# Performance work log

Hardware: AMD Instinct MI355X
Metric: run time of the kernel (lower is better)

The kernel has to match this reference:

```python
import jax, jax.numpy as jnp
import numpy as np

B, S, D = 2, 2048, 2048
H, HKV, DH = 32, 8, 64
WIN = 1024  # sliding_window
SCALE = 1.0 / np.sqrt(DH)
NEG_INF = -1e30


def setup_inputs() -> dict:
    key = jax.random.key(0)
    ks = jax.random.split(key, 6)
    w = 0.02
    inp = {
        "hidden_states": jax.random.normal(ks[0], (B, S, D), jnp.float32),
        "Wq": jax.random.normal(ks[1], (D, D), jnp.float32) * w,
        "bq": jnp.zeros((D,), jnp.float32),
        "Wk": jax.random.normal(ks[2], (HKV * DH, D), jnp.float32) * w,
        "bk": jnp.zeros((HKV * DH,), jnp.float32),
        "Wv": jax.random.normal(ks[3], (HKV * DH, D), jnp.float32) * w,
        "bv": jnp.zeros((HKV * DH,), jnp.float32),
        "Wo": jax.random.normal(ks[4], (D, D), jnp.float32) * w,
        "bo": jnp.zeros((D,), jnp.float32),
        # reset_parameters (default init): 1 / logspace(0, 7, H, base=2)
        "alibi_slopes": 1.0 / jnp.exp2(jnp.linspace(0.0, 7.0, H)).astype(jnp.float32),
    }
    return inp


def reference(hidden_states, Wq, bq, Wk, bk, Wv, bv, Wo, bo, alibi_slopes):
    x = hidden_states
    q = (x @ Wq.T + bq).reshape(B, S, H, DH).transpose(0, 2, 1, 3)      # [B,H,S,DH]
    k = (x @ Wk.T + bk).reshape(B, S, HKV, DH).transpose(0, 2, 1, 3)    # [B,HKV,S,DH]
    v = (x @ Wv.T + bv).reshape(B, S, HKV, DH).transpose(0, 2, 1, 3)
    # GQA: each kv head serves H//HKV consecutive query heads
    group = H // HKV
    k = jnp.repeat(k, group, axis=1)  # [B,H,S,DH]
    v = jnp.repeat(v, group, axis=1)

    scores = jnp.einsum("bhqd,bhkd->bhqk", q, k) * SCALE  # [B,H,S,S]
    i = jnp.arange(S)[:, None]
    j = jnp.arange(S)[None, :]
    rel = (j - i).astype(jnp.float32)  # <= 0 for attended past positions
    # ALiBi: slope * (j - i) -> linear penalty on distance
    bias = alibi_slopes[:, None, None] * rel  # [H,S,S]
    mask = (j <= i) & ((i - j) < WIN)  # [S,S]
    scores = jnp.where(mask[None, None], scores + bias[None], NEG_INF)
    probs = jax.nn.softmax(scores, axis=-1)
    out = jnp.einsum("bhqk,bhkd->bhqd", probs, v)  # [B,H,S,DH]
    out = out.transpose(0, 2, 1, 3).reshape(B, S, D)
    return out @ Wo.T + bo
```

## Files before the change

kernel.cpp:

```cpp
#include <hip/hip_runtime.h>
#include <hip/hip_bf16.h>
#include <stdint.h>
#include <type_traits>

typedef unsigned short ushort_t;
typedef __bf16 bf16x8 __attribute__((ext_vector_type(8)));
typedef __bf16 bf16x4 __attribute__((ext_vector_type(4)));
typedef short s16x4 __attribute__((ext_vector_type(4)));
typedef unsigned short u16x8 __attribute__((ext_vector_type(8)));
typedef float f32x4 __attribute__((ext_vector_type(4)));

#define MFMA_BF16(a, b, c) __builtin_amdgcn_mfma_f32_16x16x32_bf16((a), (b), (c), 0, 0, 0)

#define GLD_LDS(gptr, lptr) \
    __builtin_amdgcn_global_load_lds((const __attribute__((address_space(1))) void*)(gptr), \
                                     (__attribute__((address_space(3))) void*)(lptr), 16, 0, 0)

static __device__ __forceinline__ float bf2f(__hip_bfloat16 x) { return __bfloat162float(x); }
static __device__ __forceinline__ ushort_t f2bfbits(float f) {
    __hip_bfloat16 h = __float2bfloat16(f);
    return *(ushort_t*)&h;
}

static __device__ __forceinline__ f32x4 MFMA16(bf16x4 a, bf16x4 b, f32x4 c) {
#if __has_builtin(__builtin_amdgcn_mfma_f32_16x16x16_bf16)
    return __builtin_amdgcn_mfma_f32_16x16x16_bf16(a, b, c, 0, 0, 0);
#elif __has_builtin(__builtin_amdgcn_mfma_f32_16x16x16bf16_1k)
    union { bf16x4 b4; s16x4 s4; } ua, ub;
    ua.b4 = a; ub.b4 = b;
    return __builtin_amdgcn_mfma_f32_16x16x16bf16_1k(ua.s4, ub.s4, c, 0, 0, 0);
#else
    const bf16x4 z = {(__bf16)0.f, (__bf16)0.f, (__bf16)0.f, (__bf16)0.f};
    bf16x8 a8 = __builtin_shufflevector(a, z, 0, 1, 2, 3, 4, 5, 6, 7);
    bf16x8 b8 = __builtin_shufflevector(b, z, 0, 1, 2, 3, 4, 5, 6, 7);
    return MFMA_BF16(a8, b8, c);
#endif
}

static __device__ __forceinline__ bf16x4 pack4(float a, float b, float c, float d) {
    union { ushort4 u; bf16x4 v; } r;
    r.u = make_ushort4(f2bfbits(a), f2bfbits(b), f2bfbits(c), f2bfbits(d));
    return r.v;
}

template <typename T>
static __device__ __forceinline__ void storeT(T* p, float v);
template <>
__device__ __forceinline__ void storeT<float>(float* p, float v) { *p = v; }
template <>
__device__ __forceinline__ void storeT<__hip_bfloat16>(__hip_bfloat16* p, float v) {
    *p = __float2bfloat16(v);
}

__global__ void detect_kernel(const ushort_t* __restrict__ X,
                              const void* bq, const void* bk, const void* bv,
                              const void* bo, const void* slopes,
                              int* flag, float* slopesF, float* bqF,
                              float* bkF, float* bvF, float* boF) {
    __shared__ int cnt_s;
    if (threadIdx.x == 0) cnt_s = 0;
    __syncthreads();
    int cnt = 0;
    for (int i = threadIdx.x; i < 8192; i += 256) {
        ushort_t u = X[2 * i];
        int ex = (u >> 7) & 0xFF;
        if (ex >= 0xC0) cnt++;
    }
    for (int off = 1; off < 64; off <<= 1) cnt += __shfl_xor(cnt, off);
    if ((threadIdx.x & 63) == 0) atomicAdd(&cnt_s, cnt);
    __syncthreads();
    const bool f32 = cnt_s > 100;
    if (threadIdx.x == 0) *flag = f32 ? 1 : 0;
    auto conv = [&](const void* src, float* dst, int n) {
        for (int i = threadIdx.x; i < n; i += 256)
            dst[i] = f32 ? ((const float*)src)[i]
                         : __bfloat162float(((const __hip_bfloat16*)src)[i]);
    };
    conv(bq, bqF, 2048);
    conv(bk, bkF, 512);
    conv(bv, bvF, 512);
    conv(bo, boF, 2048);
    conv(slopes, slopesF, 32);
}

__global__ __launch_bounds__(256) void cvt_kernel(const int* __restrict__ flag,
                                                  const void* __restrict__ src,
                                                  ushort_t* __restrict__ dst, int n4) {
    const bool f32 = (*flag == 1);
    const int stride = gridDim.x * 256;
    for (int i = blockIdx.x * 256 + threadIdx.x; i < n4; i += stride) {
        if (f32) {
            float4 f = ((const float4*)src)[i];
            ((ushort4*)dst)[i] =
                make_ushort4(f2bfbits(f.x), f2bfbits(f.y), f2bfbits(f.z), f2bfbits(f.w));
        } else {
            ((ushort4*)dst)[i] = ((const ushort4*)src)[i];
        }
    }
}

__device__ __forceinline__ void stage_tile(const __hip_bfloat16* __restrict__ M, int K,
                                           int k0, ushort_t* lds, int tid) {
    const int wave = tid >> 6, lane = tid & 63;
    const int srow = lane >> 3;
    const int scol = ((lane & 7) ^ srow) * 8;
#pragma unroll
    for (int t = 0; t < 4; ++t) {
        const int chunk = wave * 4 + t;
        GLD_LDS((const ushort_t*)M + (size_t)(chunk * 8 + srow) * K + k0 + scol,
                lds + chunk * 512);
    }
}

__device__ __forceinline__ void stage_tile(const float* __restrict__ M, int K,
                                           int k0, ushort_t* lds, int tid) {
#pragma unroll
    for (int q = 0; q < 8; ++q) {
        const int idx = q * 256 + tid;
        const int row = idx >> 4;
        const int c4 = (idx & 15) * 4;
        float4 f = *(const float4*)(M + (size_t)row * K + k0 + c4);
        const int dcol = (((c4 >> 3) ^ (row & 7)) * 8) + (c4 & 7);
        *(ushort4*)(lds + row * 64 + dcol) =
            make_ushort4(f2bfbits(f.x), f2bfbits(f.y), f2bfbits(f.z), f2bfbits(f.w));
    }
}

template <typename TA, typename TW, typename TC>
__device__ __forceinline__ void gemm_tile(const TA* __restrict__ A,
                                          const TW* __restrict__ W,
                                          const float* __restrict__ biasF,
                                          TC* __restrict__ C, int K, int ldc) {
    __shared__ __align__(16) ushort_t As[128 * 64];
    __shared__ __align__(16) ushort_t Bs[128 * 64];
    const int tid = threadIdx.x;
    const int wave = tid >> 6, lane = tid & 63;
    const int quad = lane >> 4, l15 = lane & 15;
    const int wm = (wave >> 1) * 64, wn = (wave & 1) * 64;
    const int sw = l15 & 7;

    f32x4 acc[4][4];
#pragma unroll
    for (int i = 0; i < 4; ++i)
#pragma unroll
        for (int j = 0; j < 4; ++j) acc[i][j] = {0.f, 0.f, 0.f, 0.f};

    for (int k0 = 0; k0 < K; k0 += 64) {
        stage_tile(A, K, k0, As, tid);
        stage_tile(W, K, k0, Bs, tid);
        __syncthreads();
#pragma unroll
        for (int kk = 0; kk < 2; ++kk) {
            const int chs = ((kk * 4 + quad) ^ sw) * 8;
            bf16x8 af[4], bfr[4];
#pragma unroll
            for (int mi = 0; mi < 4; ++mi)
                af[mi] = *(const bf16x8*)(As + (wm + mi * 16 + l15) * 64 + chs);
#pragma unroll
            for (int ni = 0; ni < 4; ++ni)
                bfr[ni] = *(const bf16x8*)(Bs + (wn + ni * 16 + l15) * 64 + chs);
#pragma unroll
            for (int mi = 0; mi < 4; ++mi)
#pragma unroll
                for (int ni = 0; ni < 4; ++ni)
                    acc[mi][ni] = MFMA_BF16(af[mi], bfr[ni], acc[mi][ni]);
        }
        __syncthreads();
    }
#pragma unroll
    for (int mi = 0; mi < 4; ++mi) {
#pragma unroll
        for (int ni = 0; ni < 4; ++ni) {
            const int col = wn + ni * 16 + l15;
            const float bv = biasF[col];
#pragma unroll
            for (int r = 0; r < 4; ++r) {
                const int row = wm + mi * 16 + quad * 4 + r;
                storeT(C + (size_t)row * ldc + col, acc[mi][ni][r] + bv);
            }
        }
    }
}

__global__ __launch_bounds__(256, 2) void qkv_fast(
    const __hip_bfloat16* __restrict__ X,
    const __hip_bfloat16* __restrict__ Wq, const __hip_bfloat16* __restrict__ Wk,
    const __hip_bfloat16* __restrict__ Wv, const float* __restrict__ bqF,
    const float* __restrict__ bkF, const float* __restrict__ bvF,
    __hip_bfloat16* __restrict__ Qb, __hip_bfloat16* __restrict__ Kb,
    __hip_bfloat16* __restrict__ Vb) {
    const int nt = blockIdx.x, mt = blockIdx.y;
    const __hip_bfloat16* W;
    const float* bias;
    __hip_bfloat16* C;
    int ldc, colbase;
    if (nt < 16)      { W = Wq; bias = bqF; C = Qb; ldc = 2048; colbase = nt * 128; }
    else if (nt < 20) { W = Wk; bias = bkF; C = Kb; ldc = 512;  colbase = (nt - 16) * 128; }
    else              { W = Wv; bias = bvF; C = Vb; ldc = 512;  colbase = (nt - 20) * 128; }
    gemm_tile(X + (size_t)mt * 128 * 2048, W + (size_t)colbase * 2048, bias + colbase,
              C + (size_t)mt * 128 * ldc + colbase, 2048, ldc);
}

__global__ __launch_bounds__(256, 2) void oproj_fast(
    const __hip_bfloat16* __restrict__ A, const __hip_bfloat16* __restrict__ Wo,
    const float* __restrict__ boF, float* __restrict__ C) {
    gemm_tile(A + (size_t)blockIdx.y * 128 * 2048,
              Wo + (size_t)blockIdx.x * 128 * 2048, boF + blockIdx.x * 128,
              C + (size_t)blockIdx.y * 128 * 2048 + blockIdx.x * 128, 2048, 2048);
}

__global__ __launch_bounds__(256) void vtrans_kernel(const ushort_t* __restrict__ Vb,
                                                     ushort_t* __restrict__ Vt) {
    const int blk = blockIdx.x;
    const int bh = blk >> 6;
    const int sc = blk & 63;
    const int tid = threadIdx.x;
    const int dh = tid & 63;
    const int s0 = sc * 32 + (tid >> 6) * 8;
    const int b = bh >> 3, hkv = bh & 7;
    u16x8 vv;
#pragma unroll
    for (int e = 0; e < 8; ++e)
        vv[e] = Vb[((size_t)(b * 2048 + s0 + e)) * 512 + hkv * 64 + dh];
    *(u16x8*)(Vt + ((size_t)(bh * 64 + dh)) * 2048 + s0) = vv;
}

template <bool F32>
__global__ __launch_bounds__(256, 2) void qkv_kernel(
    const int* __restrict__ flag, const void* __restrict__ Xv,
    const void* __restrict__ Wqv, const void* __restrict__ Wkv,
    const void* __restrict__ Wvv, const float* __restrict__ bqF,
    const float* __restrict__ bkF, const float* __restrict__ bvF,
    __hip_bfloat16* __restrict__ Qb, __hip_bfloat16* __restrict__ Kb,
    __hip_bfloat16* __restrict__ Vb) {
    if ((*flag == 1) != F32) return;
    using T = typename std::conditional<F32, float, __hip_bfloat16>::type;
    const T* X = (const T*)Xv;
    const int nt = blockIdx.x, mt = blockIdx.y;
    const T* W;
    const float* bias;
    __hip_bfloat16* C;
    int ldc, colbase;
    if (nt < 16)      { W = (const T*)Wqv; bias = bqF; C = Qb; ldc = 2048; colbase = nt * 128; }
    else if (nt < 20) { W = (const T*)Wkv; bias = bkF; C = Kb; ldc = 512;  colbase = (nt - 16) * 128; }
    else              { W = (const T*)Wvv; bias = bvF; C = Vb; ldc = 512;  colbase = (nt - 20) * 128; }
    gemm_tile(X + (size_t)mt * 128 * 2048, W + (size_t)colbase * 2048, bias + colbase,
              C + (size_t)mt * 128 * ldc + colbase, 2048, ldc);
}

template <bool F32>
__global__ __launch_bounds__(256, 2) void oproj_kernel(
    const int* __restrict__ flag, const __hip_bfloat16* __restrict__ A,
    const void* __restrict__ Wov, const float* __restrict__ boF,
    float* __restrict__ C) {
    if ((*flag == 1) != F32) return;
    using T = typename std::conditional<F32, float, __hip_bfloat16>::type;
    gemm_tile(A + (size_t)blockIdx.y * 128 * 2048,
              (const T*)Wov + (size_t)blockIdx.x * 128 * 2048, boF + blockIdx.x * 128,
              C + (size_t)blockIdx.y * 128 * 2048 + blockIdx.x * 128, 2048, 2048);
}

__global__ __launch_bounds__(256, 4) void attn4_kernel(
    const __hip_bfloat16* __restrict__ Qg, const __hip_bfloat16* __restrict__ Kg,
    const ushort_t* __restrict__ Vt, const float* __restrict__ slopesF,
    __hip_bfloat16* __restrict__ Og) {
    constexpr int S = 2048, WIN = 1024;
    constexpr float LOG2E = 1.44269504f;
    constexpr float SCALE2 = 0.125f * LOG2E;
    constexpr float NEGBIG = -3e38f;
    __shared__ __align__(16) ushort_t K0s[64 * 64];
    __shared__ __align__(16) ushort_t V0s[64 * 64];
    __shared__ __align__(16) ushort_t K1s[64 * 64];
    __shared__ __align__(16) ushort_t V1s[64 * 64];

    const int p = blockIdx.x;
    const int xcd = p & 7;
    const int slot = p >> 3;
    const int bh = (slot >> 7) * 8 + xcd;
    const int h2 = (slot >> 5) & 3;
    const int qt = slot & 31;
    const int b = bh >> 3, hkv = bh & 7;
    const int h = hkv * 4 + h2;
    const int i0 = qt * 64;

    const int tid = threadIdx.x;
    const int wave = tid >> 6, lane = tid & 63;
    const int quad = lane >> 4, l15 = lane & 15;
    const int jl = lane >> 3, cc = lane & 7;
    const float slope2 = slopesF[h] * LOG2E;

    const ushort_t* kbase = (const ushort_t*)Kg + (size_t)(b * S) * 512 + hkv * 64;
    const ushort_t* vbase = Vt + ((size_t)bh * 64) * 2048;

    auto stage = [&](int j0, ushort_t* Ks, ushort_t* Vs) {
        const int row0 = wave * 16;
#pragma unroll
        for (int t = 0; t < 2; ++t) {
            const int r = row0 + t * 8 + jl;
            GLD_LDS(kbase + (size_t)(j0 + r) * 512 + ((cc ^ (r & 7)) * 8),
                    Ks + (row0 + t * 8) * 64);
            GLD_LDS(vbase + (size_t)r * 2048 + j0 + ((cc ^ (r & 7)) * 8),
                    Vs + (row0 + t * 8) * 64);
        }
    };

    const int i = i0 + wave * 16 + l15;
    const __hip_bfloat16* qbase = Qg + ((size_t)(b * S + i)) * 2048 + h * 64;
    bf16x8 aq0 = *(const bf16x8*)(qbase + quad * 8);
    bf16x8 aq1 = *(const bf16x8*)(qbase + 32 + quad * 8);

    f32x4 oaccT[4];
#pragma unroll
    for (int ni = 0; ni < 4; ++ni) oaccT[ni] = {0.f, 0.f, 0.f, 0.f};
    float m_i = -1e30f, l_i = 0.f;

    auto compute = [&](int j0, const ushort_t* Ks, const ushort_t* Vs, bool masked) {
        f32x4 st[4];
#pragma unroll
        for (int ni = 0; ni < 4; ++ni) st[ni] = {0.f, 0.f, 0.f, 0.f};
#pragma unroll
        for (int kk = 0; kk < 2; ++kk) {
            const bf16x8 aqk = kk ? aq1 : aq0;
#pragma unroll
            for (int ni = 0; ni < 4; ++ni) {
                const int row = ni * 16 + l15;
                bf16x8 kf = *(const bf16x8*)(Ks + row * 64 + ((kk * 4 + quad) ^ (row & 7)) * 8);
                st[ni] = MFMA_BF16(kf, aqk, st[ni]);
            }
        }
        float sv[4][4];
#pragma unroll
        for (int ni = 0; ni < 4; ++ni)
#pragma unroll
            for (int r = 0; r < 4; ++r) {
                const int rel = (j0 + ni * 16 + quad * 4 + r) - i;
                sv[ni][r] = fmaf(st[ni][r], SCALE2, slope2 * (float)rel);
            }
        if (masked) {
#pragma unroll
            for (int ni = 0; ni < 4; ++ni)
#pragma unroll
                for (int r = 0; r < 4; ++r) {
                    const int rel = (j0 + ni * 16 + quad * 4 + r) - i;
                    if (!((unsigned)(-rel) < (unsigned)WIN)) sv[ni][r] = NEGBIG;
                }
        }
        float mx = sv[0][0];
#pragma unroll
        for (int ni = 0; ni < 4; ++ni)
#pragma unroll
            for (int r = 0; r < 4; ++r) mx = fmaxf(mx, sv[ni][r]);
        mx = fmaxf(mx, __shfl_xor(mx, 16));
        mx = fmaxf(mx, __shfl_xor(mx, 32));
        const float mn = fmaxf(m_i, mx);
        const float alpha = exp2f(m_i - mn);
        m_i = mn;
        float pv[4][4];
        float rs = 0.f;
#pragma unroll
        for (int ni = 0; ni < 4; ++ni)
#pragma unroll
            for (int r = 0; r < 4; ++r) {
                pv[ni][r] = exp2f(sv[ni][r] - mn);
                rs += pv[ni][r];
            }
        rs += __shfl_xor(rs, 16);
        rs += __shfl_xor(rs, 32);
        l_i = l_i * alpha + rs;
#pragma unroll
        for (int ni = 0; ni < 4; ++ni)
#pragma unroll
            for (int r = 0; r < 4; ++r) oaccT[ni][r] *= alpha;
        bf16x4 pf[4];
#pragma unroll
        for (int c = 0; c < 4; ++c) pf[c] = pack4(pv[c][0], pv[c][1], pv[c][2], pv[c][3]);
#pragma unroll
        for (int ni = 0; ni < 4; ++ni) {
            const int row = ni * 16 + l15;
#pragma unroll
            for (int c = 0; c < 4; ++c) {
                const int cj = c * 2 + (quad >> 1);
                bf16x4 vf = *(const bf16x4*)(Vs + row * 64 + ((cj ^ (row & 7)) * 8) +
                                             (quad & 1) * 4);
                oaccT[ni] = MFMA16(vf, pf[c], oaccT[ni]);
            }
        }
    };

    const int jt_lo = (i0 - WIN + 1) > 0 ? ((i0 - WIN + 1) >> 6) : 0;
    int jt = jt_lo;
    stage(jt * 64, K0s, V0s);
    for (;;) {
        __syncthreads();
        if (jt < qt) stage((jt + 1) * 64, K1s, V1s);
        compute(jt * 64, K0s, V0s, (jt == qt) || (qt - jt >= 16));
        if (++jt > qt) break;
        __syncthreads();
        if (jt < qt) stage((jt + 1) * 64, K0s, V0s);
        compute(jt * 64, K1s, V1s, (jt == qt) || (qt - jt >= 16));
        if (++jt > qt) break;
    }
    const float inv = 1.0f / l_i;
    __hip_bfloat16* obase = Og + ((size_t)(b * S + i)) * 2048 + h * 64;
#pragma unroll
    for (int ni = 0; ni < 4; ++ni) {
        ushort4 o4 = make_ushort4(f2bfbits(oaccT[ni][0] * inv), f2bfbits(oaccT[ni][1] * inv),
                                  f2bfbits(oaccT[ni][2] * inv), f2bfbits(oaccT[ni][3] * inv));
        *(ushort4*)((ushort_t*)obase + ni * 16 + quad * 4) = o4;
    }
}

__global__ __launch_bounds__(256, 2) void attn_kernel(
    const __hip_bfloat16* __restrict__ Qg, const __hip_bfloat16* __restrict__ Kg,
    const __hip_bfloat16* __restrict__ Vg, const float* __restrict__ slopesF,
    __hip_bfloat16* __restrict__ Og) {
    constexpr int S = 2048, WIN = 1024;
    constexpr float SCALE = 0.125f;
    constexpr float LOG2E = 1.44269504f;
    __shared__ __align__(16) ushort_t P_lds[64 * 72];
    __shared__ __align__(16) ushort_t Vts[64 * 72];

    const int tile = blockIdx.x;
    const int qt = tile & 31;
    const int h = (tile >> 5) & 31;
    const int b = tile >> 10;
    const int i0 = qt * 64;
    const int hkv = h >> 2;
    const int tid = threadIdx.x;
    const int wave = tid >> 6, lane = tid & 63;
    const int quad = lane >> 4, l15 = lane & 15;
    const float slope = slopesF[h];

    const int qrow = i0 + wave * 16 + l15;
    const __hip_bfloat16* qbase = Qg + ((size_t)(b * S + qrow)) * 2048 + h * 64;
    bf16x8 aq[2];
    aq[0] = *(const bf16x8*)(qbase + quad * 8);
    aq[1] = *(const bf16x8*)(qbase + 32 + quad * 8);

    f32x4 oacc[4];
#pragma unroll
    for (int ni = 0; ni < 4; ++ni) oacc[ni] = {0.f, 0.f, 0.f, 0.f};
    float m_i[4], l_i[4];
#pragma unroll
    for (int r = 0; r < 4; ++r) { m_i[r] = -1e30f; l_i[r] = 0.f; }

    const int jt_lo = (i0 - WIN + 1) > 0 ? ((i0 - WIN + 1) >> 6) : 0;
    for (int jt = jt_lo; jt <= qt; ++jt) {
        const int j0 = jt * 64;
#pragma unroll
        for (int it = 0; it < 2; ++it) {
            const int j = it * 32 + (tid >> 3);
            const int dh0 = (tid & 7) * 8;
            u16x8 vv = *(const u16x8*)(Vg + ((size_t)(b * S + j0 + j)) * 512 + hkv * 64 + dh0);
#pragma unroll
            for (int e = 0; e < 8; ++e) Vts[(dh0 + e) * 72 + j] = vv[e];
        }
        f32x4 sacc[4];
#pragma unroll
        for (int ni = 0; ni < 4; ++ni) sacc[ni] = {0.f, 0.f, 0.f, 0.f};
#pragma unroll
        for (int kk = 0; kk < 2; ++kk) {
#pragma unroll
            for (int ni = 0; ni < 4; ++ni) {
                bf16x8 bkf = *(const bf16x8*)(Kg + ((size_t)(b * S + j0 + ni * 16 + l15)) * 512 +
                                              hkv * 64 + kk * 32 + quad * 8);
                sacc[ni] = MFMA_BF16(aq[kk], bkf, sacc[ni]);
            }
        }
#pragma unroll
        for (int r = 0; r < 4; ++r) {
            const int i = i0 + wave * 16 + quad * 4 + r;
            float sv[4];
            float rowmax = -1e30f;
#pragma unroll
            for (int ni = 0; ni < 4; ++ni) {
                const int j = j0 + ni * 16 + l15;
                float s = sacc[ni][r] * SCALE + slope * (float)(j - i);
                const bool valid = (j <= i) && ((i - j) < WIN);
                s = valid ? s : -1e30f;
                sv[ni] = s;
                rowmax = fmaxf(rowmax, s);
            }
#pragma unroll
            for (int off = 1; off < 16; off <<= 1)
                rowmax = fmaxf(rowmax, __shfl_xor(rowmax, off));
            const float mn = fmaxf(m_i[r], rowmax);
            const float alpha = exp2f((m_i[r] - mn) * LOG2E);
            float rowsum = 0.f;
#pragma unroll
            for (int ni = 0; ni < 4; ++ni) {
                const float p = (sv[ni] > -1e29f) ? exp2f((sv[ni] - mn) * LOG2E) : 0.f;
                P_lds[(wave * 16 + quad * 4 + r) * 72 + ni * 16 + l15] = f2bfbits(p);
                rowsum += p;
            }
#pragma unroll
            for (int off = 1; off < 16; off <<= 1) rowsum += __shfl_xor(rowsum, off);
            l_i[r] = l_i[r] * alpha + rowsum;
            m_i[r] = mn;
#pragma unroll
            for (int ni = 0; ni < 4; ++ni) oacc[ni][r] *= alpha;
        }
        __syncthreads();
#pragma unroll
        for (int kk = 0; kk < 2; ++kk) {
            bf16x8 ap = *(const bf16x8*)(P_lds + (wave * 16 + l15) * 72 + kk * 32 + quad * 8);
#pragma unroll
            for (int ni = 0; ni < 4; ++ni) {
                bf16x8 bvf = *(const bf16x8*)(Vts + (ni * 16 + l15) * 72 + kk * 32 + quad * 8);
                oacc[ni] = MFMA_BF16(ap, bvf, oacc[ni]);
            }
        }
        __syncthreads();
    }
#pragma unroll
    for (int ni = 0; ni < 4; ++ni) {
#pragma unroll
        for (int r = 0; r < 4; ++r) {
            const int srow = i0 + wave * 16 + quad * 4 + r;
            const float v = oacc[ni][r] / l_i[r];
            Og[((size_t)(b * S + srow)) * 2048 + h * 64 + ni * 16 + l15] = __float2bfloat16(v);
        }
    }
}

extern "C" void kernel_launch(void* const* d_in, const int* in_sizes, int n_in,
                              void* d_out, int out_size, void* d_ws, size_t ws_size,
                              hipStream_t stream) {
    (void)in_sizes; (void)n_in; (void)out_size;
    const void* X  = d_in[0];
    const void* Wq = d_in[1];
    const void* bq = d_in[2];
    const void* Wk = d_in[3];
    const void* bk = d_in[4];
    const void* Wv = d_in[5];
    const void* bv = d_in[6];
    const void* Wo = d_in[7];
    const void* bo = d_in[8];
    const void* sl = d_in[9];
    float* outp = (float*)d_out;

    char* ws = (char*)d_ws;
    const size_t SZ_X  = (size_t)4096 * 2048 * 2;
    const size_t SZ_WQ = (size_t)2048 * 2048 * 2;
    const size_t SZ_WK = (size_t)512 * 2048 * 2;
    const size_t SZ_Q  = SZ_X;
    const size_t SZ_K  = (size_t)4096 * 512 * 2;
    const size_t FAST_NEED = SZ_X + SZ_WQ + 2 * SZ_WK + SZ_Q + 2 * SZ_K + 65536;

    if (ws_size >= FAST_NEED) {
        size_t o = 0;
        __hip_bfloat16* Xb  = (__hip_bfloat16*)(ws + o); o += SZ_X;
        __hip_bfloat16* Wqb = (__hip_bfloat16*)(ws + o); o += SZ_WQ;
        __hip_bfloat16* Wkb = (__hip_bfloat16*)(ws + o); o += SZ_WK;
        __hip_bfloat16* Wvb = (__hip_bfloat16*)(ws + o); o += SZ_WK;
        __hip_bfloat16* Qb  = (__hip_bfloat16*)(ws + o); o += SZ_Q;
        __hip_bfloat16* Kb  = (__hip_bfloat16*)(ws + o); o += SZ_K;
        __hip_bfloat16* Vb  = (__hip_bfloat16*)(ws + o); o += SZ_K;
        __hip_bfloat16* Ab  = Xb;
        __hip_bfloat16* Wob = Wqb;
        ushort_t*       Vtg = (ushort_t*)Wkb;
        int*   flag    = (int*)(ws + o);
        float* slopesF = (float*)(ws + o + 1024);
        float* bqF     = (float*)(ws + o + 4096);
        float* bkF     = bqF + 2048;
        float* bvF     = bkF + 512;
        float* boF     = bvF + 512;

        detect_kernel<<<1, 256, 0, stream>>>((const ushort_t*)X, bq, bk, bv, bo, sl,
                                             flag, slopesF, bqF, bkF, bvF, boF);
        cvt_kernel<<<2048, 256, 0, stream>>>(flag, X,  (ushort_t*)Xb,  4096 * 2048 / 4);
        cvt_kernel<<<2048, 256, 0, stream>>>(flag, Wq, (ushort_t*)Wqb, 2048 * 2048 / 4);
        cvt_kernel<<<512,  256, 0, stream>>>(flag, Wk, (ushort_t*)Wkb, 512 * 2048 / 4);
        cvt_kernel<<<512,  256, 0, stream>>>(flag, Wv, (ushort_t*)Wvb, 512 * 2048 / 4);
        qkv_fast<<<dim3(24, 32), 256, 0, stream>>>(Xb, Wqb, Wkb, Wvb, bqF, bkF, bvF,
                                                   Qb, Kb, Vb);
        vtrans_kernel<<<1024, 256, 0, stream>>>((const ushort_t*)Vb, Vtg);
        cvt_kernel<<<2048, 256, 0, stream>>>(flag, Wo, (ushort_t*)Wob, 2048 * 2048 / 4);
        attn4_kernel<<<dim3(2048), 256, 0, stream>>>(Qb, Kb, Vtg, slopesF, Ab);
        oproj_fast<<<dim3(16, 32), 256, 0, stream>>>(Ab, Wob, boF, outp);
    } else {
        const size_t MB = 1024 * 1024;
        __hip_bfloat16* Qb = (__hip_bfloat16*)(ws);
        __hip_bfloat16* Kb = (__hip_bfloat16*)(ws + 16 * MB);
        __hip_bfloat16* Vb = (__hip_bfloat16*)(ws + 20 * MB);
        __hip_bfloat16* Ab = (__hip_bfloat16*)(ws + 24 * MB);
        int*   flag    = (int*)(ws + 40 * MB);
        float* slopesF = (float*)(ws + 40 * MB + 1024);
        float* bqF     = (float*)(ws + 40 * MB + 4096);
        float* bkF     = bqF + 2048;
        float* bvF     = bkF + 512;
        float* boF     = bvF + 512;

        detect_kernel<<<1, 256, 0, stream>>>((const ushort_t*)X, bq, bk, bv, bo, sl,
                                             flag, slopesF, bqF, bkF, bvF, boF);
        qkv_kernel<false><<<dim3(24, 32), 256, 0, stream>>>(flag, X, Wq, Wk, Wv,
                                                            bqF, bkF, bvF, Qb, Kb, Vb);
        qkv_kernel<true><<<dim3(24, 32), 256, 0, stream>>>(flag, X, Wq, Wk, Wv,
                                                           bqF, bkF, bvF, Qb, Kb, Vb);
        attn_kernel<<<dim3(2048), 256, 0, stream>>>(Qb, Kb, Vb, slopesF, Ab);
        oproj_kernel<false><<<dim3(16, 32), 256, 0, stream>>>(flag, Ab, Wo, boF, outp);
        oproj_kernel<true><<<dim3(16, 32), 256, 0, stream>>>(flag, Ab, Wo, boF, outp);
    }
}
```

Before: 337.8 us.

## Use 256x256 eight-wave ping-pong GEMM tiles for QKV and output projections

```diff
diff --git a/kernel.cpp b/kernel.cpp
--- a/kernel.cpp
+++ b/kernel.cpp
@@ -15,6 +15,38 @@
 #define GLD_LDS(gptr, lptr) \
     __builtin_amdgcn_global_load_lds((const __attribute__((address_space(1))) void*)(gptr), \
                                      (__attribute__((address_space(3))) void*)(lptr), 16, 0, 0)
+
+#define WAIT_VM(n) asm volatile("s_waitcnt vmcnt(" #n ")" ::: "memory")
+#define WAIT_LGKM0 asm volatile("s_waitcnt lgkmcnt(0)" ::: "memory")
+#define SCHED0 __builtin_amdgcn_sched_barrier(0)
+#define SBAR __builtin_amdgcn_s_barrier()
+
+#define PH_SYNC()      \
+    do {               \
+        SCHED0;        \
+        SBAR;          \
+        WAIT_LGKM0;    \
+        SCHED0;        \
+    } while (0)
+#define PH_END() \
+    do {         \
+        SCHED0;  \
+        SBAR;    \
+    } while (0)
+
+#define MFMA_QUAD(M0, N0)                                                               \
+    do {                                                                                \
+        __builtin_amdgcn_s_setprio(1);                                                  \
+        _Pragma("unroll") for (int mi_ = 0; mi_ < 4; ++mi_) {                           \
+            _Pragma("unroll") for (int ni_ = 0; ni_ < 2; ++ni_) {                       \
+                _Pragma("unroll") for (int kk_ = 0; kk_ < 2; ++kk_) {                   \
+                    acc[(M0) + mi_][(N0) + ni_] = MFMA_BF16(                            \
+                        af[mi_][kk_], bfr[(N0) + ni_][kk_], acc[(M0) + mi_][(N0) + ni_]); \
+                }                                                                       \
+            }                                                                           \
+        }                                                                               \
+        __builtin_amdgcn_s_setprio(0);                                                  \
+    } while (0)
 
 static __device__ __forceinline__ float bf2f(__hip_bfloat16 x) { return __bfloat162float(x); }
 static __device__ __forceinline__ ushort_t f2bfbits(float f) {
@@ -182,7 +214,200 @@
     }
 }
 
-__global__ __launch_bounds__(256, 2) void qkv_fast(
+__device__ __forceinline__ void stage_half(const ushort_t* __restrict__ G, int ldg,
+                                           int row0, int k0, ushort_t* lds) {
+    const int tid = threadIdx.x;
+    const int wave = tid >> 6, lane = tid & 63;
+    const int rl = lane >> 3, c = lane & 7;
+#pragma unroll
+    for (int rd = 0; rd < 2; ++rd) {
+        const int r = rd * 64 + wave * 8 + rl;
+        GLD_LDS(G + (size_t)(row0 + r) * ldg + (k0 + ((c ^ rl) * 8)),
+                lds + rd * 4096 + wave * 512);
+    }
+}
+
+template <typename TC>
+__device__ __forceinline__ void gemm256_tile(const __hip_bfloat16* __restrict__ A,
+                                             const __hip_bfloat16* __restrict__ W,
+                                             const float* __restrict__ biasF,
+                                             TC* __restrict__ C, int K, int ldc) {
+    __shared__ __align__(16) ushort_t As[2 * 256 * 64];
+    __shared__ __align__(16) ushort_t Bs[2 * 256 * 64];
+    const ushort_t* Au = (const ushort_t*)A;
+    const ushort_t* Wu = (const ushort_t*)W;
+    const int tid = threadIdx.x;
+    const int lane = tid & 63;
+    const int wave = tid >> 6;
+    const int quad = lane >> 4, l15 = lane & 15;
+    const int wm = (wave >> 2) * 128;
+    const int wn = (wave & 3) * 64;
+
+    f32x4 acc[8][4];
+#pragma unroll
+    for (int i = 0; i < 8; ++i)
+#pragma unroll
+        for (int j = 0; j < 4; ++j) acc[i][j] = {0.f, 0.f, 0.f, 0.f};
+
+    auto stageA = [&](int buf, int tile, int half) {
+        stage_half(Au, K, half * 128, tile * 64, As + buf * 16384 + half * 8192);
+    };
+    auto stageB = [&](int buf, int tile, int half) {
+        stage_half(Wu, K, half * 128, tile * 64, Bs + buf * 16384 + half * 8192);
+    };
+
+    stageB(0, 0, 0);
+    stageB(0, 0, 1);
+    stageA(0, 0, 0);
+    stageA(0, 0, 1);
+    stageB(1, 1, 0);
+    stageB(1, 1, 1);
+    WAIT_VM(4);
+    SBAR;
+
+    bf16x8 af[4][2], bfr[4][2];
+    const int NI = K >> 7;
+    for (int it = 0; it < NI; ++it) {
+        const int t0 = it * 2;
+        const bool nl = (it != NI - 1);
+
+        {
+            const ushort_t* Ab = As;
+            const ushort_t* Bb = Bs;
+#pragma unroll
+            for (int mi = 0; mi < 4; ++mi) {
+                const int R = wm + mi * 16 + l15;
+#pragma unroll
+                for (int kk = 0; kk < 2; ++kk)
+                    af[mi][kk] =
+                        *(const bf16x8*)(Ab + R * 64 + (((kk * 4 + quad) ^ (R & 7)) * 8));
+            }
+#pragma unroll
+            for (int ni = 0; ni < 2; ++ni) {
+                const int R = wn + ni * 16 + l15;
+#pragma unroll
+                for (int kk = 0; kk < 2; ++kk)
+                    bfr[ni][kk] =
+                        *(const bf16x8*)(Bb + R * 64 + (((kk * 4 + quad) ^ (R & 7)) * 8));
+            }
+            stageA(1, t0 + 1, 0);
+            PH_SYNC();
+            MFMA_QUAD(0, 0);
+            PH_END();
+
+#pragma unroll
+            for (int ni = 2; ni < 4; ++ni) {
+                const int R = wn + ni * 16 + l15;
+#pragma unroll
+                for (int kk = 0; kk < 2; ++kk)
+                    bfr[ni][kk] =
+                        *(const bf16x8*)(Bb + R * 64 + (((kk * 4 + quad) ^ (R & 7)) * 8));
+            }
+            stageA(1, t0 + 1, 1);
+            PH_SYNC();
+            MFMA_QUAD(0, 2);
+            PH_END();
+
+#pragma unroll
+            for (int mi = 0; mi < 4; ++mi) {
+                const int R = wm + (mi + 4) * 16 + l15;
+#pragma unroll
+                for (int kk = 0; kk < 2; ++kk)
+                    af[mi][kk] =
+                        *(const bf16x8*)(Ab + R * 64 + (((kk * 4 + quad) ^ (R & 7)) * 8));
+            }
+            if (nl) stageB(0, t0 + 2, 0);
+            PH_SYNC();
+            MFMA_QUAD(4, 0);
+            PH_END();
+
+            if (nl) {
+                stageB(0, t0 + 2, 1);
+                WAIT_VM(4);
+            } else {
+                WAIT_VM(0);
+            }
+            PH_SYNC();
+            MFMA_QUAD(4, 2);
+            PH_END();
+        }
+
+        {
+            const ushort_t* Ab = As + 16384;
+            const ushort_t* Bb = Bs + 16384;
+#pragma unroll
+            for (int mi = 0; mi < 4; ++mi) {
+                const int R = wm + mi * 16 + l15;
+#pragma unroll
+                for (int kk = 0; kk < 2; ++kk)
+                    af[mi][kk] =
+                        *(const bf16x8*)(Ab + R * 64 + (((kk * 4 + quad) ^ (R & 7)) * 8));
+            }
+#pragma unroll
+            for (int ni = 0; ni < 2; ++ni) {
+                const int R = wn + ni * 16 + l15;
+#pragma unroll
+                for (int kk = 0; kk < 2; ++kk)
+                    bfr[ni][kk] =
+                        *(const bf16x8*)(Bb + R * 64 + (((kk * 4 + quad) ^ (R & 7)) * 8));
+            }
+            if (nl) stageA(0, t0 + 2, 0);
+            PH_SYNC();
+            MFMA_QUAD(0, 0);
+            PH_END();
+
+#pragma unroll
+            for (int ni = 2; ni < 4; ++ni) {
+                const int R = wn + ni * 16 + l15;
+#pragma unroll
+                for (int kk = 0; kk < 2; ++kk)
+                    bfr[ni][kk] =
+                        *(const bf16x8*)(Bb + R * 64 + (((kk * 4 + quad) ^ (R & 7)) * 8));
+            }
+            if (nl) stageA(0, t0 + 2, 1);
+            PH_SYNC();
+            MFMA_QUAD(0, 2);
+            PH_END();
+
+#pragma unroll
+            for (int mi = 0; mi < 4; ++mi) {
+                const int R = wm + (mi + 4) * 16 + l15;
+#pragma unroll
+                for (int kk = 0; kk < 2; ++kk)
+                    af[mi][kk] =
+                        *(const bf16x8*)(Ab + R * 64 + (((kk * 4 + quad) ^ (R & 7)) * 8));
+            }
+            if (nl) stageB(1, t0 + 3, 0);
+            PH_SYNC();
+            MFMA_QUAD(4, 0);
+            PH_END();
+
+            if (nl) {
+                stageB(1, t0 + 3, 1);
+                WAIT_VM(4);
+            }
+            PH_SYNC();
+            MFMA_QUAD(4, 2);
+            PH_END();
+        }
+    }
+
+#pragma unroll
+    for (int mi = 0; mi < 8; ++mi) {
+#pragma unroll
+        for (int ni = 0; ni < 4; ++ni) {
+            const int col = wn + ni * 16 + l15;
+            const float bv = biasF[col];
+#pragma unroll
+            for (int r = 0; r < 4; ++r) {
+                const int row = wm + mi * 16 + quad * 4 + r;
+                storeT(C + (size_t)row * ldc + col, acc[mi][ni][r] + bv);
+            }
+        }
+    }
+}
+
+__global__ __launch_bounds__(512, 2) void qkv_fast8(
     const __hip_bfloat16* __restrict__ X,
     const __hip_bfloat16* __restrict__ Wq, const __hip_bfloat16* __restrict__ Wk,
     const __hip_bfloat16* __restrict__ Wv, const float* __restrict__ bqF,
@@ -194,19 +419,19 @@
     const float* bias;
     __hip_bfloat16* C;
     int ldc, colbase;
-    if (nt < 16)      { W = Wq; bias = bqF; C = Qb; ldc = 2048; colbase = nt * 128; }
-    else if (nt < 20) { W = Wk; bias = bkF; C = Kb; ldc = 512;  colbase = (nt - 16) * 128; }
-    else              { W = Wv; bias = bvF; C = Vb; ldc = 512;  colbase = (nt - 20) * 128; }
-    gemm_tile(X + (size_t)mt * 128 * 2048, W + (size_t)colbase * 2048, bias + colbase,
-              C + (size_t)mt * 128 * ldc + colbase, 2048, ldc);
-}
-
-__global__ __launch_bounds__(256, 2) void oproj_fast(
+    if (nt < 8)       { W = Wq; bias = bqF; C = Qb; ldc = 2048; colbase = nt * 256; }
+    else if (nt < 10) { W = Wk; bias = bkF; C = Kb; ldc = 512;  colbase = (nt - 8) * 256; }
+    else              { W = Wv; bias = bvF; C = Vb; ldc = 512;  colbase = (nt - 10) * 256; }
+    gemm256_tile(X + (size_t)mt * 256 * 2048, W + (size_t)colbase * 2048, bias + colbase,
+                 C + (size_t)mt * 256 * ldc + colbase, 2048, ldc);
+}
+
+__global__ __launch_bounds__(512, 2) void oproj_fast8(
     const __hip_bfloat16* __restrict__ A, const __hip_bfloat16* __restrict__ Wo,
     const float* __restrict__ boF, float* __restrict__ C) {
-    gemm_tile(A + (size_t)blockIdx.y * 128 * 2048,
-              Wo + (size_t)blockIdx.x * 128 * 2048, boF + blockIdx.x * 128,
-              C + (size_t)blockIdx.y * 128 * 2048 + blockIdx.x * 128, 2048, 2048);
+    gemm256_tile(A + (size_t)blockIdx.y * 256 * 2048,
+                 Wo + (size_t)blockIdx.x * 256 * 2048, boF + blockIdx.x * 256,
+                 C + (size_t)blockIdx.y * 256 * 2048 + blockIdx.x * 256, 2048, 2048);
 }
 
 __global__ __launch_bounds__(256) void vtrans_kernel(const ushort_t* __restrict__ Vb,
@@ -572,12 +797,12 @@
         cvt_kernel<<<2048, 256, 0, stream>>>(flag, Wq, (ushort_t*)Wqb, 2048 * 2048 / 4);
         cvt_kernel<<<512,  256, 0, stream>>>(flag, Wk, (ushort_t*)Wkb, 512 * 2048 / 4);
         cvt_kernel<<<512,  256, 0, stream>>>(flag, Wv, (ushort_t*)Wvb, 512 * 2048 / 4);
-        qkv_fast<<<dim3(24, 32), 256, 0, stream>>>(Xb, Wqb, Wkb, Wvb, bqF, bkF, bvF,
-                                                   Qb, Kb, Vb);
+        qkv_fast8<<<dim3(12, 16), 512, 0, stream>>>(Xb, Wqb, Wkb, Wvb, bqF, bkF, bvF,
+                                                    Qb, Kb, Vb);
         vtrans_kernel<<<1024, 256, 0, stream>>>((const ushort_t*)Vb, Vtg);
         cvt_kernel<<<2048, 256, 0, stream>>>(flag, Wo, (ushort_t*)Wob, 2048 * 2048 / 4);
         attn4_kernel<<<dim3(2048), 256, 0, stream>>>(Qb, Kb, Vtg, slopesF, Ab);
-        oproj_fast<<<dim3(16, 32), 256, 0, stream>>>(Ab, Wob, boF, outp);
+        oproj_fast8<<<dim3(8, 16), 512, 0, stream>>>(Ab, Wob, boF, outp);
     } else {
         const size_t MB = 1024 * 1024;
         __hip_bfloat16* Qb = (__hip_bfloat16*)(ws);
```

Measured after the change: 348.5 us. 3.2% more time.

## Lazy softmax rescale, MFMA row-sum, reversed tile order in attention

Applied to the files above, without the earlier changes.

```diff
diff --git a/kernel.cpp b/kernel.cpp
--- a/kernel.cpp
+++ b/kernel.cpp
@@ -20,6 +20,9 @@
 static __device__ __forceinline__ ushort_t f2bfbits(float f) {
     __hip_bfloat16 h = __float2bfloat16(f);
     return *(ushort_t*)&h;
+}
+static __device__ __forceinline__ float fmax3(float a, float b, float c) {
+    return fmaxf(fmaxf(a, b), c);
 }
 
 static __device__ __forceinline__ f32x4 MFMA16(bf16x4 a, bf16x4 b, f32x4 c) {
@@ -278,7 +281,7 @@
     const int slot = p >> 3;
     const int bh = (slot >> 7) * 8 + xcd;
     const int h2 = (slot >> 5) & 3;
-    const int qt = slot & 31;
+    const int qt = 31 - (slot & 31);
     const int b = bh >> 3, hkv = bh & 7;
     const int h = hkv * 4 + h2;
     const int i0 = qt * 64;
@@ -309,10 +312,15 @@
     bf16x8 aq0 = *(const bf16x8*)(qbase + quad * 8);
     bf16x8 aq1 = *(const bf16x8*)(qbase + 32 + quad * 8);
 
+    union { ushort4 u; bf16x4 v; } onesu;
+    onesu.u = make_ushort4(0x3F80, 0x3F80, 0x3F80, 0x3F80);
+    const bf16x4 onesf = onesu.v;
+
     f32x4 oaccT[4];
 #pragma unroll
     for (int ni = 0; ni < 4; ++ni) oaccT[ni] = {0.f, 0.f, 0.f, 0.f};
-    float m_i = -1e30f, l_i = 0.f;
+    f32x4 lacc = {0.f, 0.f, 0.f, 0.f};
+    float m_i = -1e30f;
 
     auto compute = [&](int j0, const ushort_t* Ks, const ushort_t* Vs, bool masked) {
         f32x4 st[4];
@@ -345,35 +353,34 @@
                     if (!((unsigned)(-rel) < (unsigned)WIN)) sv[ni][r] = NEGBIG;
                 }
         }
-        float mx = sv[0][0];
-#pragma unroll
-        for (int ni = 0; ni < 4; ++ni)
-#pragma unroll
-            for (int r = 0; r < 4; ++r) mx = fmaxf(mx, sv[ni][r]);
+        float mx = fmax3(fmax3(sv[0][0], sv[0][1], sv[0][2]),
+                         fmax3(sv[0][3], sv[1][0], sv[1][1]),
+                         fmax3(sv[1][2], sv[1][3], sv[2][0]));
+        float my = fmax3(fmax3(sv[2][1], sv[2][2], sv[2][3]),
+                         fmax3(sv[3][0], sv[3][1], sv[3][2]), sv[3][3]);
+        mx = fmaxf(mx, my);
         mx = fmaxf(mx, __shfl_xor(mx, 16));
         mx = fmaxf(mx, __shfl_xor(mx, 32));
-        const float mn = fmaxf(m_i, mx);
-        const float alpha = exp2f(m_i - mn);
-        m_i = mn;
+        if (!__all(mx <= m_i + 8.f)) {
+            const float mn = fmaxf(m_i, mx);
+            const float alpha = exp2f(m_i - mn);
+            m_i = mn;
+#pragma unroll
+            for (int ni = 0; ni < 4; ++ni)
+#pragma unroll
+                for (int r = 0; r < 4; ++r) oaccT[ni][r] *= alpha;
+            lacc[0] *= alpha;
+        }
         float pv[4][4];
-        float rs = 0.f;
 #pragma unroll
         for (int ni = 0; ni < 4; ++ni)
 #pragma unroll
-            for (int r = 0; r < 4; ++r) {
-                pv[ni][r] = exp2f(sv[ni][r] - mn);
-                rs += pv[ni][r];
-            }
-        rs += __shfl_xor(rs, 16);
-        rs += __shfl_xor(rs, 32);
-        l_i = l_i * alpha + rs;
-#pragma unroll
-        for (int ni = 0; ni < 4; ++ni)
-#pragma unroll
-            for (int r = 0; r < 4; ++r) oaccT[ni][r] *= alpha;
+            for (int r = 0; r < 4; ++r) pv[ni][r] = exp2f(sv[ni][r] - m_i);
         bf16x4 pf[4];
 #pragma unroll
         for (int c = 0; c < 4; ++c) pf[c] = pack4(pv[c][0], pv[c][1], pv[c][2], pv[c][3]);
+#pragma unroll
+        for (int c = 0; c < 4; ++c) lacc = MFMA16(onesf, pf[c], lacc);
 #pragma unroll
         for (int ni = 0; ni < 4; ++ni) {
             const int row = ni * 16 + l15;
@@ -400,7 +407,7 @@
         compute(jt * 64, K1s, V1s, (jt == qt) || (qt - jt >= 16));
         if (++jt > qt) break;
     }
-    const float inv = 1.0f / l_i;
+    const float inv = 1.0f / lacc[0];
     __hip_bfloat16* obase = Og + ((size_t)(b * S + i)) * 2048 + h * 64;
 #pragma unroll
     for (int ni = 0; ni < 4; ++ni) {
```

Measured after the change: 340.2 us. Within noise of the previous version (+0.7%).
